# Kernel tuning notes

Measured on AMD Instinct MI355X. Metric: run time of the kernel, lower is better.

The kernel has to match this reference:

```python
import jax, jax.numpy as jnp
import numpy as np

B, S, D, H, DFF = 8, 1024, 1024, 16, 4096
DK = D // H
EPS = 1e-6
NEG = -1e9


def setup_inputs() -> dict:
    key = jax.random.key(0)
    ks = jax.random.split(key, 8)
    x = jax.random.normal(ks[0], (B, S, D), dtype=jnp.float32)
    mask = jnp.ones((B, 1, 1, S), dtype=jnp.int32)
    s = 0.02
    wq = jax.random.normal(ks[1], (D, D), jnp.float32) * s
    wk = jax.random.normal(ks[2], (D, D), jnp.float32) * s
    wv = jax.random.normal(ks[3], (D, D), jnp.float32) * s
    wo = jax.random.normal(ks[4], (D, D), jnp.float32) * s
    bq = jnp.zeros((D,), jnp.float32); bk = jnp.zeros((D,), jnp.float32)
    bv = jnp.zeros((D,), jnp.float32); bo = jnp.zeros((D,), jnp.float32)
    w1 = jax.random.normal(ks[5], (D, DFF), jnp.float32) * s
    b1 = jnp.zeros((DFF,), jnp.float32)
    w2 = jax.random.normal(ks[6], (DFF, D), jnp.float32) * s
    b2 = jnp.zeros((D,), jnp.float32)
    g1 = jnp.array(1.0, jnp.float32); be1 = jnp.array(0.0, jnp.float32)
    g2 = jnp.array(1.0, jnp.float32); be2 = jnp.array(0.0, jnp.float32)
    return dict(x=x, mask=mask, wq=wq, bq=bq, wk=wk, bk=bk, wv=wv, bv=bv,
                wo=wo, bo=bo, w1=w1, b1=b1, w2=w2, b2=b2,
                g1=g1, be1=be1, g2=g2, be2=be2)


def layer_norm(x, gamma, beta):
    # repo quirk: unbiased std (ddof=1), scalar gamma/beta, divide by (std+eps)
    mean = jnp.mean(x, axis=-1, keepdims=True)
    std = jnp.std(x, axis=-1, keepdims=True, ddof=1)
    return gamma * (x - mean) / (std + EPS) + beta


def mha(x, mask, wq, bq, wk, bk, wv, bv, wo, bo):
    q = (x @ wq + bq).reshape(B, S, H, DK).transpose(0, 2, 1, 3)  # bhsd
    k = (x @ wk + bk).reshape(B, S, H, DK).transpose(0, 2, 1, 3)
    v = (x @ wv + bv).reshape(B, S, H, DK).transpose(0, 2, 1, 3)
    scores = jnp.einsum('bhqd,bhkd->bhqk', q, k) / jnp.sqrt(jnp.float32(DK))
    scores = jnp.where(mask == 0, NEG, scores)
    attn = jax.nn.softmax(scores, axis=-1)
    out = jnp.einsum('bhqk,bhkd->bhqd', attn, v)
    out = out.transpose(0, 2, 1, 3).reshape(B, S, D)
    return out @ wo + bo


def reference(x, mask, wq, bq, wk, bk, wv, bv, wo, bo, w1, b1, w2, b2, g1, be1, g2, be2):
    # pre-LN residual: x + sublayer(norm(x)); dropout inert at eval
    x = x + mha(layer_norm(x, g1, be1), mask, wq, bq, wk, bk, wv, bv, wo, bo)
    h = layer_norm(x, g2, be2)
    x = x + (jax.nn.relu(h @ w1 + b1) @ w2 + b2)
    return x
```

## Files before the change

### kernel.cpp

```cpp
#include <hip/hip_runtime.h>
#include <math.h>

typedef __bf16 bf16;
typedef float f32x4 __attribute__((ext_vector_type(4)));
typedef float f32x16 __attribute__((ext_vector_type(16)));
typedef bf16 bf16x8 __attribute__((ext_vector_type(8)));
typedef bf16 bf16x4 __attribute__((ext_vector_type(4)));
typedef unsigned int u32;
typedef unsigned int u32x2 __attribute__((ext_vector_type(2)));

#define DEV __device__ __forceinline__

constexpr int Ss = 1024, Dd = 1024;
constexpr float EPSf = 1e-6f;
constexpr float SM_SCALE = 0.125f * 1.4426950408889634f;

DEV void gl_lds16(const void* g, void* l) {
  __builtin_amdgcn_global_load_lds(
      (const __attribute__((address_space(1))) void*)g,
      (__attribute__((address_space(3))) void*)l, 16, 0, 0);
}

DEV u32 cvtpk(float lo, float hi) {
  u32 r;
  asm("v_cvt_pk_bf16_f32 %0, %1, %2" : "=v"(r) : "v"(lo), "v"(hi));
  return r;
}

__global__ __launch_bounds__(256) void prep_k(
    const float* __restrict__ i0, const float* __restrict__ i1,
    const float* __restrict__ i2, const float* __restrict__ i3,
    const float* __restrict__ i4, const float* __restrict__ i5,
    bf16* __restrict__ o0, bf16* __restrict__ o1, bf16* __restrict__ o2,
    bf16* __restrict__ o3, bf16* __restrict__ o4, bf16* __restrict__ o5,
    const float* __restrict__ xin, bf16* __restrict__ lnout,
    const float* __restrict__ gp, const float* __restrict__ bp) {
  const int bi = blockIdx.x;
  const int tid = threadIdx.x;
  if (bi >= 3072) {
    const int row = bi - 3072;
    float v[4];
    const float* p = xin + (size_t)row * Dd + tid * 4;
#pragma unroll
    for (int i = 0; i < 4; i++) v[i] = p[i];
    float s = v[0] + v[1] + v[2] + v[3];
    float s2 = v[0] * v[0] + v[1] * v[1] + v[2] * v[2] + v[3] * v[3];
#pragma unroll
    for (int m = 1; m < 64; m <<= 1) {
      s += __shfl_xor(s, m, 64);
      s2 += __shfl_xor(s2, m, 64);
    }
    __shared__ float ls[4], ls2[4];
    if ((tid & 63) == 0) {
      ls[tid >> 6] = s;
      ls2[tid >> 6] = s2;
    }
    __syncthreads();
    s = ls[0] + ls[1] + ls[2] + ls[3];
    s2 = ls2[0] + ls2[1] + ls2[2] + ls2[3];
    float mean = s * (1.0f / Dd);
    float var = (s2 - (float)Dd * mean * mean) * (1.0f / (Dd - 1));
    var = fmaxf(var, 0.0f);
    float g = gp[0], be = bp[0];
    float rs = g / (sqrtf(var) + EPSf);
    bf16* q = lnout + (size_t)row * Dd + tid * 4;
#pragma unroll
    for (int i = 0; i < 4; i++) q[i] = (bf16)((v[i] - mean) * rs + be);
    return;
  }
  __shared__ float t[64 * 65];
  const float* in;
  bf16* out;
  int R, C, local, sh;
  if (bi < 1024) {
    const int j = bi >> 8;
    local = bi & 255; R = 1024; C = 1024; sh = 4;
    in = (j == 0) ? i0 : (j == 1) ? i1 : (j == 2) ? i2 : i3;
    out = (j == 0) ? o0 : (j == 1) ? o1 : (j == 2) ? o2 : o3;
  } else if (bi < 2048) {
    local = bi - 1024; R = 1024; C = 4096; sh = 6; in = i4; out = o4;
  } else {
    local = bi - 2048; R = 4096; C = 1024; sh = 4; in = i5; out = o5;
  }
  const int nx = 1 << sh;
  const int bx = local & (nx - 1), by = local >> sh;
  const int tx = tid & 63, ty = tid >> 6;
  const int r0 = by * 64, c0 = bx * 64;
#pragma unroll
  for (int i = 0; i < 16; i++) {
    int r = ty + i * 4;
    t[r * 65 + tx] = in[(size_t)(r0 + r) * C + c0 + tx];
  }
  __syncthreads();
#pragma unroll
  for (int i = 0; i < 16; i++) {
    int r = ty + i * 4;
    out[(size_t)(c0 + r) * R + r0 + tx] = (bf16)t[tx * 65 + r];
  }
}

__global__ __launch_bounds__(256) void ln_bf16_k(
    const bf16* __restrict__ in, bf16* __restrict__ out,
    const float* __restrict__ gp, const float* __restrict__ bp) {
  const int row = blockIdx.x;
  const int tid = threadIdx.x;
  const bf16x4 vv = *(const bf16x4*)(in + (size_t)row * Dd + tid * 4);
  float v[4];
#pragma unroll
  for (int i = 0; i < 4; i++) v[i] = (float)vv[i];
  float s = v[0] + v[1] + v[2] + v[3];
  float s2 = v[0] * v[0] + v[1] * v[1] + v[2] * v[2] + v[3] * v[3];
#pragma unroll
  for (int m = 1; m < 64; m <<= 1) {
    s += __shfl_xor(s, m, 64);
    s2 += __shfl_xor(s2, m, 64);
  }
  __shared__ float ls[4], ls2[4];
  if ((tid & 63) == 0) {
    ls[tid >> 6] = s;
    ls2[tid >> 6] = s2;
  }
  __syncthreads();
  s = ls[0] + ls[1] + ls[2] + ls[3];
  s2 = ls2[0] + ls2[1] + ls2[2] + ls2[3];
  float mean = s * (1.0f / Dd);
  float var = (s2 - (float)Dd * mean * mean) * (1.0f / (Dd - 1));
  var = fmaxf(var, 0.0f);
  float g = gp[0], be = bp[0];
  float rs = g / (sqrtf(var) + EPSf);
  bf16* q = out + (size_t)row * Dd + tid * 4;
#pragma unroll
  for (int i = 0; i < 4; i++) q[i] = (bf16)((v[i] - mean) * rs + be);
}

template <int EPI, int BK>
__global__ __launch_bounds__(256) void gemm_bt(
    const bf16* __restrict__ A, const bf16* __restrict__ Bt,
    const float* __restrict__ bias, const float* __restrict__ bias2,
    const float* __restrict__ bias3, const float* __restrict__ resid,
    const bf16* __restrict__ vtbr, bf16* __restrict__ vtb,
    void* __restrict__ Cout, int M, int N, int K, int sa, int sb) {
  __shared__ __attribute__((aligned(16))) char smem[2 * 128 * BK * 2];
  bf16* As = (bf16*)smem;
  bf16* Bs = (bf16*)(smem + 128 * BK * 2);
  constexpr int CPR = BK / 8;
  constexpr int RPJ = 256 / CPR;
  constexpr int NJ = BK / 16;
  const int tid = threadIdx.x;
  const int ln = tid & 63;
  const int wv = tid >> 6;
  const int wm = wv >> 1, wn = wv & 1;
  const int quad = ln >> 4, l16 = ln & 15;
  const int l7 = l16 & 7;
  const int nxg = gridDim.x;
  const int d = blockIdx.y * nxg + blockIdx.x;
  const int sseq = d >> 3;
  const int bxr = sseq % nxg;
  const int byr = (d & 7) + 8 * (sseq / nxg);
  const int m0 = byr * 128, n0 = bxr * 128;

  f32x4 acc[4][4];
#pragma unroll
  for (int i = 0; i < 4; i++)
#pragma unroll
    for (int j = 0; j < 4; j++) acc[i][j] = {0.f, 0.f, 0.f, 0.f};

  const int sr = tid / CPR;
  const int sc = (tid & (CPR - 1)) ^ (sr & 7);
  const size_t abase = (size_t)(m0 + sr) * sa + sc * 8;
  const size_t bbase = (size_t)(n0 + sr) * sb + sc * 8;

  for (int k0 = 0; k0 < K; k0 += BK) {
#pragma unroll
    for (int j = 0; j < NJ; j++) {
      gl_lds16(A + abase + (size_t)(j * RPJ) * sa + k0,
               (char*)As + j * 4096 + wv * 1024);
      gl_lds16(Bt + bbase + (size_t)(j * RPJ) * sb + k0,
               (char*)Bs + j * 4096 + wv * 1024);
    }
    __syncthreads();
#pragma unroll
    for (int kh = 0; kh < BK / 32; kh++) {
      bf16x8 af[4], bfr[4];
#pragma unroll
      for (int mi = 0; mi < 4; mi++)
        af[mi] = *(const bf16x8*)&As[(wm * 64 + mi * 16 + l16) * BK +
                                     ((kh * 4 + quad) ^ l7) * 8];
#pragma unroll
      for (int ni = 0; ni < 4; ni++)
        bfr[ni] = *(const bf16x8*)&Bs[(wn * 64 + ni * 16 + l16) * BK +
                                      ((kh * 4 + quad) ^ l7) * 8];
#pragma unroll
      for (int mi = 0; mi < 4; mi++)
#pragma unroll
        for (int ni = 0; ni < 4; ni++)
          acc[mi][ni] = __builtin_amdgcn_mfma_f32_16x16x32_bf16(
              af[mi], bfr[ni], acc[mi][ni], 0, 0, 0);
    }
    __syncthreads();
  }

  if constexpr (EPI == 4) {
    if (n0 < 2048) {
#pragma unroll
      for (int mi = 0; mi < 4; mi++) {
        const int m = m0 + wm * 64 + mi * 16 + quad * 4;
#pragma unroll
        for (int ni = 0; ni < 4; ni++) {
          const int n = n0 + wn * 64 + ni * 16 + l16;
          const float bvl = (n < 1024) ? bias[n] : bias2[n - 1024];
#pragma unroll
          for (int r = 0; r < 4; r++)
            ((bf16*)Cout)[(size_t)(m + r) * N + n] =
                (bf16)(acc[mi][ni][r] + bvl);
        }
      }
    } else {
      bf16* T = (bf16*)smem;
#pragma unroll
      for (int mi = 0; mi < 4; mi++) {
        const int ml = wm * 64 + mi * 16 + quad * 4;
        const int c = ml >> 3, hf = (ml >> 2) & 1;
#pragma unroll
        for (int ni = 0; ni < 4; ni++) {
          const int nl = wn * 64 + ni * 16 + l16;
          const float bvl = bias3[(n0 - 2048) + nl];
          bf16x4 tv;
#pragma unroll
          for (int r = 0; r < 4; r++) tv[r] = (bf16)(acc[mi][ni][r] + bvl);
          *(bf16x4*)&T[nl * 128 + ((c ^ (nl & 15)) << 3) + (hf << 2)] = tv;
        }
      }
      __syncthreads();
      const size_t vbase =
          ((size_t)(m0 >> 10) * 1024 + (n0 - 2048)) * Ss + (m0 & 1023);
#pragma unroll
      for (int p = 0; p < 8; p++) {
        const int row = p * 16 + (tid >> 4);
        const int k = tid & 15;
        bf16x8 vv = *(const bf16x8*)&T[row * 128 + ((k ^ (row & 15)) << 3)];
        *(bf16x8*)&vtb[vbase + (size_t)row * Ss + k * 8] = vv;
      }
    }
  } else {
#pragma unroll
    for (int mi = 0; mi < 4; mi++) {
      const int m = m0 + wm * 64 + mi * 16 + quad * 4;
#pragma unroll
      for (int ni = 0; ni < 4; ni++) {
        const int n = n0 + wn * 64 + ni * 16 + l16;
        float bvl = 0.0f;
        if constexpr (EPI != 3) bvl = bias[n];
#pragma unroll
        for (int r = 0; r < 4; r++) {
          float val = acc[mi][ni][r] + bvl;
          const size_t idx = (size_t)(m + r) * N + n;
          if constexpr (EPI == 1) {
            ((float*)Cout)[idx] = val + resid[idx];
          } else if constexpr (EPI == 2) {
            ((bf16*)Cout)[idx] = (bf16)fmaxf(val, 0.0f);
          } else if constexpr (EPI == 3) {
            ((float*)Cout)[idx] = val + resid[idx];
          } else if constexpr (EPI == 5) {
            ((bf16*)Cout)[idx] = (bf16)(val + resid[idx]);
          } else {
            ((float*)Cout)[idx] = val + (float)vtbr[idx];
          }
        }
      }
    }
  }
}

__global__ __launch_bounds__(512) void gemm256_relu(
    const bf16* __restrict__ A, const bf16* __restrict__ Bt,
    const float* __restrict__ bias, bf16* __restrict__ Cout, int M, int N,
    int K, int sa, int sb) {
  __shared__ __attribute__((aligned(16))) char smem[131072];
  const int tid = threadIdx.x;
  const int ln = tid & 63;
  const int wv = tid >> 6;
  const int wm = wv >> 2, wn = wv & 3;
  const int quad = ln >> 4, l16 = ln & 15;
  const int l7 = l16 & 7;
  const int nxg = gridDim.x;
  const int d = blockIdx.y * nxg + blockIdx.x;
  const int sseq = d >> 3;
  const int bxr = sseq % nxg;
  const int byr = (d & 7) + 8 * (sseq / nxg);
  const int m0 = byr * 256, n0 = bxr * 256;

  f32x4 acc[8][4];
#pragma unroll
  for (int i = 0; i < 8; i++)
#pragma unroll
    for (int j = 0; j < 4; j++) acc[i][j] = {0.f, 0.f, 0.f, 0.f};

  const int sr = tid >> 3;
  const int sc = (tid & 7) ^ (sr & 7);
  const size_t abase = (size_t)(m0 + sr) * sa + sc * 8;
  const size_t bbase = (size_t)(n0 + sr) * sb + sc * 8;
  const int w8 = tid >> 6;

  const int nt = K >> 6;
  int cur = 0;

  {
#pragma unroll
    for (int j = 0; j < 4; j++) {
      gl_lds16(A + abase + (size_t)(j * 64) * sa,
               smem + j * 8192 + w8 * 1024);
      gl_lds16(Bt + bbase + (size_t)(j * 64) * sb,
               smem + 32768 + j * 8192 + w8 * 1024);
    }
  }
  asm volatile("s_waitcnt vmcnt(0)" ::: "memory");
  __builtin_amdgcn_s_barrier();

  for (int t = 0; t < nt; ++t) {
    const bf16* As = (const bf16*)(smem + cur * 65536);
    const bf16* Bs = (const bf16*)(smem + cur * 65536 + 32768);
    char* ldst = smem + (cur ^ 1) * 65536;
    const bool pf = (t + 1 < nt);
    const int koff = (t + 1) * 64;

    bf16x8 af0[4][2], af1[4][2], bfr[2][2];

#pragma unroll
    for (int mf = 0; mf < 4; mf++)
#pragma unroll
      for (int kh = 0; kh < 2; kh++)
        af0[mf][kh] = *(const bf16x8*)&As[(wm * 128 + mf * 16 + l16) * 64 +
                                          (((kh * 4 + quad) ^ l7) * 8)];
#pragma unroll
    for (int nf = 0; nf < 2; nf++)
#pragma unroll
      for (int kh = 0; kh < 2; kh++)
        bfr[nf][kh] = *(const bf16x8*)&Bs[(wn * 64 + nf * 16 + l16) * 64 +
                                          (((kh * 4 + quad) ^ l7) * 8)];
    if (pf) {
      gl_lds16(Bt + bbase + koff, ldst + 32768 + w8 * 1024);
      gl_lds16(Bt + bbase + (size_t)64 * sb + koff,
               ldst + 32768 + 8192 + w8 * 1024);
    }
    __builtin_amdgcn_s_barrier();
    __builtin_amdgcn_s_setprio(1);
#pragma unroll
    for (int kh = 0; kh < 2; kh++)
#pragma unroll
      for (int mf = 0; mf < 4; mf++)
#pragma unroll
        for (int nf = 0; nf < 2; nf++)
          acc[mf][nf] = __builtin_amdgcn_mfma_f32_16x16x32_bf16(
              af0[mf][kh], bfr[nf][kh], acc[mf][nf], 0, 0, 0);
    __builtin_amdgcn_s_setprio(0);
    if (pf) {
      asm volatile("s_waitcnt vmcnt(2)" ::: "memory");
    } else {
      asm volatile("s_waitcnt vmcnt(0)" ::: "memory");
    }
    __builtin_amdgcn_s_barrier();

#pragma unroll
    for (int mf = 0; mf < 4; mf++)
#pragma unroll
      for (int kh = 0; kh < 2; kh++)
        af1[mf][kh] =
            *(const bf16x8*)&As[(wm * 128 + 64 + mf * 16 + l16) * 64 +
                                (((kh * 4 + quad) ^ l7) * 8)];
    if (pf) {
      gl_lds16(Bt + bbase + (size_t)128 * sb + koff,
               ldst + 32768 + 16384 + w8 * 1024);
      gl_lds16(Bt + bbase + (size_t)192 * sb + koff,
               ldst + 32768 + 24576 + w8 * 1024);
    }
    __builtin_amdgcn_s_barrier();
    __builtin_amdgcn_s_setprio(1);
#pragma unroll
    for (int kh = 0; kh < 2; kh++)
#pragma unroll
      for (int mf = 0; mf < 4; mf++)
#pragma unroll
        for (int nf = 0; nf < 2; nf++)
          acc[4 + mf][nf] = __builtin_amdgcn_mfma_f32_16x16x32_bf16(
              af1[mf][kh], bfr[nf][kh], acc[4 + mf][nf], 0, 0, 0);
    __builtin_amdgcn_s_setprio(0);
    __builtin_amdgcn_s_barrier();

#pragma unroll
    for (int nf = 0; nf < 2; nf++)
#pragma unroll
      for (int kh = 0; kh < 2; kh++)
        bfr[nf][kh] =
            *(const bf16x8*)&Bs[(wn * 64 + 32 + nf * 16 + l16) * 64 +
                                (((kh * 4 + quad) ^ l7) * 8)];
    if (pf) {
      gl_lds16(A + abase + koff, ldst + w8 * 1024);
      gl_lds16(A + abase + (size_t)128 * sa + koff,
               ldst + 16384 + w8 * 1024);
    }
    __builtin_amdgcn_s_barrier();
    __builtin_amdgcn_s_setprio(1);
#pragma unroll
    for (int kh = 0; kh < 2; kh++)
#pragma unroll
      for (int mf = 0; mf < 4; mf++)
#pragma unroll
        for (int nf = 0; nf < 2; nf++)
          acc[4 + mf][2 + nf] = __builtin_amdgcn_mfma_f32_16x16x32_bf16(
              af1[mf][kh], bfr[nf][kh], acc[4 + mf][2 + nf], 0, 0, 0);
    __builtin_amdgcn_s_setprio(0);
    __builtin_amdgcn_s_barrier();

    if (pf) {
      gl_lds16(A + abase + (size_t)64 * sa + koff, ldst + 8192 + w8 * 1024);
      gl_lds16(A + abase + (size_t)192 * sa + koff,
               ldst + 24576 + w8 * 1024);
    }
    __builtin_amdgcn_s_barrier();
    __builtin_amdgcn_s_setprio(1);
#pragma unroll
    for (int kh = 0; kh < 2; kh++)
#pragma unroll
      for (int mf = 0; mf < 4; mf++)
#pragma unroll
        for (int nf = 0; nf < 2; nf++)
          acc[mf][2 + nf] = __builtin_amdgcn_mfma_f32_16x16x32_bf16(
              af0[mf][kh], bfr[nf][kh], acc[mf][2 + nf], 0, 0, 0);
    __builtin_amdgcn_s_setprio(0);
    if (pf) {
      asm volatile("s_waitcnt vmcnt(2)" ::: "memory");
    } else {
      asm volatile("s_waitcnt vmcnt(0)" ::: "memory");
    }
    __builtin_amdgcn_s_barrier();
    cur ^= 1;
  }

#pragma unroll
  for (int mi = 0; mi < 8; mi++) {
    const int m = m0 + wm * 128 + mi * 16 + quad * 4;
#pragma unroll
    for (int ni = 0; ni < 4; ni++) {
      const int n = n0 + wn * 64 + ni * 16 + l16;
      const float bvl = bias[n];
#pragma unroll
      for (int r = 0; r < 4; r++)
        Cout[(size_t)(m + r) * N + n] =
            (bf16)fmaxf(acc[mi][ni][r] + bvl, 0.0f);
    }
  }
}

__global__ __launch_bounds__(256) void attn_k(
    const bf16* __restrict__ qkv, const bf16* __restrict__ vt,
    const int* __restrict__ mask, bf16* __restrict__ ctx) {
  __shared__ __attribute__((aligned(16))) char smem[36864];
  __shared__ int Ft[16];
  bf16* Qs = (bf16*)smem;
  float* Fm = (float*)(smem + 32768);
  const int tid = threadIdx.x;
  const int l = tid & 63, w = tid >> 6;
  const int lq = l & 31, lh = l >> 5;
  const int lq7 = lq & 7;
  const int bh = blockIdx.x;
  const int b = bh >> 4, h = bh & 15;
  const int q0 = blockIdx.y * 128;
  const int sr = tid >> 3;
  const int sc = (tid & 7) ^ (sr & 7);

  if (tid < 16) Ft[tid] = 0;
  {
#pragma unroll
    for (int j = 0; j < 4; j++) {
      const size_t ga =
          (size_t)(b * Ss + q0 + j * 32 + sr) * 3072 + h * 64 + sc * 8;
      gl_lds16(qkv + ga, smem + j * 4096 + w * 1024);
    }
#pragma unroll
    for (int j = 0; j < 2; j++) {
      const size_t ga =
          (size_t)(b * Ss + j * 32 + sr) * 3072 + 1024 + h * 64 + sc * 8;
      gl_lds16(qkv + ga, smem + 16384 + j * 4096 + w * 1024);
      const size_t gv = (size_t)(bh * 64 + j * 32 + sr) * Ss + sc * 8;
      gl_lds16(vt + gv, smem + 24576 + j * 4096 + w * 1024);
    }
  }
  {
    const int4 mv = *(const int4*)&mask[b * Ss + tid * 4];
    const float ninf = -__builtin_inff();
    Fm[tid * 4 + 0] = mv.x ? 0.0f : ninf;
    Fm[tid * 4 + 1] = mv.y ? 0.0f : ninf;
    Fm[tid * 4 + 2] = mv.z ? 0.0f : ninf;
    Fm[tid * 4 + 3] = mv.w ? 0.0f : ninf;
    if (!(mv.x && mv.y && mv.z && mv.w)) atomicOr(&Ft[tid >> 4], 1);
  }
  __syncthreads();

  bf16x8 qf[4];
#pragma unroll
  for (int s = 0; s < 4; s++)
    qf[s] =
        *(const bf16x8*)&Qs[(w * 32 + lq) * 64 + (((s * 2 + lh) ^ lq7) * 8)];
  __syncthreads();

  f32x16 oacc[2];
#pragma unroll
  for (int d = 0; d < 2; d++)
#pragma unroll
    for (int r = 0; r < 16; r++) oacc[d][r] = 0.0f;
  float rsum = 0.0f;

  for (int t = 0; t < 16; ++t) {
    const int kk0 = t * 64;
    if (t + 1 < 16) {
      char* dst = smem + (((t + 1) & 1) ? 0 : 16384);
      const int nk = kk0 + 64;
#pragma unroll
      for (int j = 0; j < 2; j++) {
        const size_t ga =
            (size_t)(b * Ss + nk + j * 32 + sr) * 3072 + 1024 + h * 64 +
            sc * 8;
        gl_lds16(qkv + ga, dst + j * 4096 + w * 1024);
        const size_t gv = (size_t)(bh * 64 + j * 32 + sr) * Ss + nk + sc * 8;
        gl_lds16(vt + gv, dst + 8192 + j * 4096 + w * 1024);
      }
      asm volatile("s_waitcnt vmcnt(4)" ::: "memory");
    } else {
      asm volatile("s_waitcnt vmcnt(0)" ::: "memory");
    }
    __builtin_amdgcn_s_barrier();
    const bf16* Ks = (const bf16*)(smem + ((t & 1) ? 0 : 16384));
    const bf16* Vs = Ks + 4096;

    f32x16 sacc[2];
#pragma unroll
    for (int kb = 0; kb < 2; kb++)
#pragma unroll
      for (int r = 0; r < 16; r++) sacc[kb][r] = 0.0f;

    __builtin_amdgcn_s_setprio(1);
#pragma unroll
    for (int kb = 0; kb < 2; kb++)
#pragma unroll
      for (int s = 0; s < 4; s++) {
        const bf16x8 kf = *(const bf16x8*)&Ks[(kb * 32 + lq) * 64 +
                                              (((s * 2 + lh) ^ lq7) * 8)];
        sacc[kb] = __builtin_amdgcn_mfma_f32_32x32x16_bf16(kf, qf[s],
                                                           sacc[kb], 0, 0, 0);
      }
    __builtin_amdgcn_s_setprio(0);

    if (__builtin_amdgcn_readfirstlane(Ft[t])) {
#pragma unroll
      for (int kb = 0; kb < 2; kb++)
#pragma unroll
        for (int g = 0; g < 4; g++) {
          const f32x4 mv = *(const f32x4*)&Fm[kk0 + kb * 32 + 4 * lh + 8 * g];
#pragma unroll
          for (int j = 0; j < 4; j++)
            sacc[kb][g * 4 + j] = __builtin_amdgcn_exp2f(
                fmaf(sacc[kb][g * 4 + j], SM_SCALE, mv[j]));
        }
    } else {
#pragma unroll
      for (int kb = 0; kb < 2; kb++)
#pragma unroll
        for (int r = 0; r < 16; r++)
          sacc[kb][r] = __builtin_amdgcn_exp2f(sacc[kb][r] * SM_SCALE);
    }
#pragma unroll
    for (int kb = 0; kb < 2; kb++) {
      const float t0 = (sacc[kb][0] + sacc[kb][1]) + (sacc[kb][2] + sacc[kb][3]);
      const float t1 = (sacc[kb][4] + sacc[kb][5]) + (sacc[kb][6] + sacc[kb][7]);
      const float t2 =
          (sacc[kb][8] + sacc[kb][9]) + (sacc[kb][10] + sacc[kb][11]);
      const float t3 =
          (sacc[kb][12] + sacc[kb][13]) + (sacc[kb][14] + sacc[kb][15]);
      rsum += ((t0 + t1) + (t2 + t3));
    }

    __builtin_amdgcn_s_setprio(1);
#pragma unroll
    for (int tt = 0; tt < 4; tt++) {
      const int kb = tt >> 1, rb = (tt & 1) * 8;
      u32 pa = cvtpk(sacc[kb][rb + 0], sacc[kb][rb + 1]);
      u32 pbv = cvtpk(sacc[kb][rb + 2], sacc[kb][rb + 3]);
      u32 pc = cvtpk(sacc[kb][rb + 4], sacc[kb][rb + 5]);
      u32 pd = cvtpk(sacc[kb][rb + 6], sacc[kb][rb + 7]);
      asm("v_permlane32_swap_b32 %0, %1" : "+v"(pa), "+v"(pc));
      asm("v_permlane32_swap_b32 %0, %1" : "+v"(pbv), "+v"(pd));
      union {
        u32 u[4];
        bf16x8 v;
      } pk;
      pk.u[0] = pa;
      pk.u[1] = pbv;
      pk.u[2] = pc;
      pk.u[3] = pd;
      const int vsw = ((tt * 2 + lh) ^ lq7) * 8;
      const bf16x8 vf0 = *(const bf16x8*)&Vs[lq * 64 + vsw];
      const bf16x8 vf1 = *(const bf16x8*)&Vs[(32 + lq) * 64 + vsw];
      oacc[0] =
          __builtin_amdgcn_mfma_f32_32x32x16_bf16(vf0, pk.v, oacc[0], 0, 0, 0);
      oacc[1] =
          __builtin_amdgcn_mfma_f32_32x32x16_bf16(vf1, pk.v, oacc[1], 0, 0, 0);
    }
    __builtin_amdgcn_s_setprio(0);
    asm volatile("s_waitcnt lgkmcnt(0)" ::: "memory");
    __builtin_amdgcn_s_barrier();
  }

  float xs = rsum, ys = rsum;
  asm("v_permlane32_swap_b32 %0, %1" : "+v"(xs), "+v"(ys));
  const float inv = 1.0f / (xs + ys);

  bf16* Tb = (bf16*)(smem + w * 4608);
#pragma unroll
  for (int dblk = 0; dblk < 2; dblk++)
#pragma unroll
    for (int g = 0; g < 4; g++) {
      const u32 lo =
          cvtpk(oacc[dblk][g * 4 + 0] * inv, oacc[dblk][g * 4 + 1] * inv);
      const u32 hi =
          cvtpk(oacc[dblk][g * 4 + 2] * inv, oacc[dblk][g * 4 + 3] * inv);
      u32x2 pr2;
      pr2[0] = lo;
      pr2[1] = hi;
      const int dbase = dblk * 32 + 8 * g + 4 * lh;
      *(u32x2*)&Tb[lq * 72 + dbase] = pr2;
    }
  __syncthreads();
#pragma unroll
  for (int p = 0; p < 4; p++) {
    const int row = p * 8 + (l >> 3);
    const int ch = l & 7;
    const bf16x8 vv = *(const bf16x8*)&Tb[row * 72 + ch * 8];
    *(bf16x8*)&ctx[(size_t)(b * Ss + q0 + w * 32 + row) * Dd + h * 64 +
                   ch * 8] = vv;
  }
}

extern "C" void kernel_launch(void* const* d_in, const int* in_sizes, int n_in,
                              void* d_out, int out_size, void* d_ws,
                              size_t ws_size, hipStream_t stream) {
  (void)in_sizes; (void)n_in; (void)out_size;
  const float* x = (const float*)d_in[0];
  const int* mask = (const int*)d_in[1];
  const float* wq = (const float*)d_in[2];
  const float* bq = (const float*)d_in[3];
  const float* wk = (const float*)d_in[4];
  const float* bk = (const float*)d_in[5];
  const float* wvw = (const float*)d_in[6];
  const float* bv = (const float*)d_in[7];
  const float* wo = (const float*)d_in[8];
  const float* bo = (const float*)d_in[9];
  const float* w1 = (const float*)d_in[10];
  const float* b1 = (const float*)d_in[11];
  const float* w2 = (const float*)d_in[12];
  const float* b2 = (const float*)d_in[13];
  const float* g1 = (const float*)d_in[14];
  const float* be1 = (const float*)d_in[15];
  const float* g2 = (const float*)d_in[16];
  const float* be2 = (const float*)d_in[17];
  float* out = (float*)d_out;

  char* ws = (char*)d_ws;
  const size_t MB = 1024 * 1024;
  bf16* w1T = (bf16*)(ws + 0 * MB);
  bf16* w2T = (bf16*)(ws + 8 * MB);
  bf16* wqkvT = (bf16*)(ws + 16 * MB);
  bf16* woT = (bf16*)(ws + 22 * MB);
  bf16* lnb = (bf16*)(ws + 24 * MB);
  bf16* qkv = (bf16*)(ws + 40 * MB);
  bf16* vtb = (bf16*)(ws + 88 * MB);
  bf16* x1b = (bf16*)(ws + 40 * MB);
  bf16* ctx = lnb;

  dim3 blk(256);
  prep_k<<<3072 + 8192, blk, 0, stream>>>(
      wq, wk, wvw, wo, w1, w2, wqkvT, wqkvT + (size_t)1024 * 1024,
      wqkvT + (size_t)2048 * 1024, woT, w1T, w2T, x, lnb, g1, be1);
  gemm_bt<4, 64><<<dim3(24, 64), blk, 0, stream>>>(
      lnb, wqkvT, bq, bk, bv, nullptr, nullptr, vtb, qkv, 8192, 3072, 1024,
      1024, 1024);
  attn_k<<<dim3(128, 8), blk, 0, stream>>>(qkv, vtb, mask, ctx);
  gemm_bt<5, 128><<<dim3(8, 64), blk, 0, stream>>>(
      ctx, woT, bo, nullptr, nullptr, x, nullptr, nullptr, x1b, 8192, 1024,
      1024, 1024, 1024);
  ln_bf16_k<<<8192, blk, 0, stream>>>(x1b, lnb, g2, be2);

  if (ws_size >= 136 * MB) {
    bf16* mid = (bf16*)(ws + 72 * MB);
    gemm256_relu<<<dim3(16, 32), dim3(512), 0, stream>>>(
        lnb, w1T, b1, mid, 8192, 4096, 1024, 1024, 1024);
    gemm_bt<6, 128><<<dim3(8, 64), blk, 0, stream>>>(
        mid, w2T, b2, nullptr, nullptr, nullptr, x1b, nullptr, out, 8192,
        1024, 4096, 4096, 4096);
  } else {
    bf16* mid = (bf16*)(ws + 72 * MB);
    gemm256_relu<<<dim3(8, 32), dim3(512), 0, stream>>>(
        lnb, w1T, b1, mid, 8192, 2048, 1024, 1024, 1024);
    gemm_bt<6, 128><<<dim3(8, 64), blk, 0, stream>>>(
        mid, w2T, b2, nullptr, nullptr, nullptr, x1b, nullptr, out, 8192,
        1024, 2048, 2048, 4096);
    gemm256_relu<<<dim3(8, 32), dim3(512), 0, stream>>>(
        lnb, w1T + (size_t)2048 * 1024, b1 + 2048, mid, 8192, 2048, 1024,
        1024, 1024);
    gemm_bt<3, 128><<<dim3(8, 64), blk, 0, stream>>>(
        mid, w2T + 2048, nullptr, nullptr, nullptr, out, nullptr, nullptr,
        out, 8192, 1024, 2048, 2048, 4096);
  }
}
```

Measured before the change: 441.0 us.

## Double-buffer LDS in gemm_bt and rebalance prefetch issue in gemm256_relu

gemm_bt now keeps two 32KB LDS stages with BK fixed at 64. It prefetches the next K tile via global_load_lds while computing on the current one, replacing the load-sync-compute-sync loop. The BK=128 launches for the Wo and W2 GEMMs switch to BK=64 to fit this layout. In gemm256_relu the prefetch loads are redistributed across the first three phases, one barrier is removed, and the vmcnt waits are adjusted. This costs 64KB of LDS per block, which may lower occupancy, and BK=64 means more loop iterations.

Result: faster. 417.1 us (-5.4%).

```diff
diff --git a/kernel.cpp b/kernel.cpp
--- a/kernel.cpp
+++ b/kernel.cpp
@@ -140,9 +140,8 @@
     const float* __restrict__ bias3, const float* __restrict__ resid,
     const bf16* __restrict__ vtbr, bf16* __restrict__ vtb,
     void* __restrict__ Cout, int M, int N, int K, int sa, int sb) {
-  __shared__ __attribute__((aligned(16))) char smem[2 * 128 * BK * 2];
-  bf16* As = (bf16*)smem;
-  bf16* Bs = (bf16*)(smem + 128 * BK * 2);
+  static_assert(BK == 64, "dbuf layout assumes BK=64");
+  __shared__ __attribute__((aligned(16))) char smem[65536];
   constexpr int CPR = BK / 8;
   constexpr int RPJ = 256 / CPR;
   constexpr int NJ = BK / 16;
@@ -170,25 +169,50 @@
   const size_t abase = (size_t)(m0 + sr) * sa + sc * 8;
   const size_t bbase = (size_t)(n0 + sr) * sb + sc * 8;
 
-  for (int k0 = 0; k0 < K; k0 += BK) {
+  const int nt = K >> 6;
+  int cur = 0;
+
+  {
 #pragma unroll
     for (int j = 0; j < NJ; j++) {
-      gl_lds16(A + abase + (size_t)(j * RPJ) * sa + k0,
-               (char*)As + j * 4096 + wv * 1024);
-      gl_lds16(Bt + bbase + (size_t)(j * RPJ) * sb + k0,
-               (char*)Bs + j * 4096 + wv * 1024);
-    }
-    __syncthreads();
-#pragma unroll
-    for (int kh = 0; kh < BK / 32; kh++) {
+      gl_lds16(A + abase + (size_t)(j * RPJ) * sa,
+               (char*)smem + j * 4096 + wv * 1024);
+      gl_lds16(Bt + bbase + (size_t)(j * RPJ) * sb,
+               (char*)smem + 16384 + j * 4096 + wv * 1024);
+    }
+  }
+  asm volatile("s_waitcnt vmcnt(0)" ::: "memory");
+  __builtin_amdgcn_s_barrier();
+
+  for (int t = 0; t < nt; ++t) {
+    if (t + 1 < nt) {
+      char* dl = smem + ((cur ^ 1) * 32768);
+      const int koff = (t + 1) * 64;
+#pragma unroll
+      for (int j = 0; j < NJ; j++) {
+        gl_lds16(A + abase + (size_t)(j * RPJ) * sa + koff,
+                 dl + j * 4096 + wv * 1024);
+        gl_lds16(Bt + bbase + (size_t)(j * RPJ) * sb + koff,
+                 dl + 16384 + j * 4096 + wv * 1024);
+      }
+      asm volatile("s_waitcnt vmcnt(8)" ::: "memory");
+    } else {
+      asm volatile("s_waitcnt vmcnt(0)" ::: "memory");
+    }
+    __builtin_amdgcn_s_barrier();
+
+    const bf16* As = (const bf16*)(smem + cur * 32768);
+    const bf16* Bs = (const bf16*)(smem + cur * 32768 + 16384);
+#pragma unroll
+    for (int kh = 0; kh < 2; kh++) {
       bf16x8 af[4], bfr[4];
 #pragma unroll
       for (int mi = 0; mi < 4; mi++)
-        af[mi] = *(const bf16x8*)&As[(wm * 64 + mi * 16 + l16) * BK +
+        af[mi] = *(const bf16x8*)&As[(wm * 64 + mi * 16 + l16) * 64 +
                                      ((kh * 4 + quad) ^ l7) * 8];
 #pragma unroll
       for (int ni = 0; ni < 4; ni++)
-        bfr[ni] = *(const bf16x8*)&Bs[(wn * 64 + ni * 16 + l16) * BK +
+        bfr[ni] = *(const bf16x8*)&Bs[(wn * 64 + ni * 16 + l16) * 64 +
                                       ((kh * 4 + quad) ^ l7) * 8];
 #pragma unroll
       for (int mi = 0; mi < 4; mi++)
@@ -197,7 +221,8 @@
           acc[mi][ni] = __builtin_amdgcn_mfma_f32_16x16x32_bf16(
               af[mi], bfr[ni], acc[mi][ni], 0, 0, 0);
     }
-    __syncthreads();
+    __builtin_amdgcn_s_barrier();
+    cur ^= 1;
   }
 
   if constexpr (EPI == 4) {
@@ -342,6 +367,8 @@
       gl_lds16(Bt + bbase + koff, ldst + 32768 + w8 * 1024);
       gl_lds16(Bt + bbase + (size_t)64 * sb + koff,
                ldst + 32768 + 8192 + w8 * 1024);
+      gl_lds16(Bt + bbase + (size_t)128 * sb + koff,
+               ldst + 32768 + 16384 + w8 * 1024);
     }
     __builtin_amdgcn_s_barrier();
     __builtin_amdgcn_s_setprio(1);
@@ -355,7 +382,7 @@
               af0[mf][kh], bfr[nf][kh], acc[mf][nf], 0, 0, 0);
     __builtin_amdgcn_s_setprio(0);
     if (pf) {
-      asm volatile("s_waitcnt vmcnt(2)" ::: "memory");
+      asm volatile("s_waitcnt vmcnt(3)" ::: "memory");
     } else {
       asm volatile("s_waitcnt vmcnt(0)" ::: "memory");
     }
@@ -369,10 +396,11 @@
             *(const bf16x8*)&As[(wm * 128 + 64 + mf * 16 + l16) * 64 +
                                 (((kh * 4 + quad) ^ l7) * 8)];
     if (pf) {
-      gl_lds16(Bt + bbase + (size_t)128 * sb + koff,
-               ldst + 32768 + 16384 + w8 * 1024);
       gl_lds16(Bt + bbase + (size_t)192 * sb + koff,
                ldst + 32768 + 24576 + w8 * 1024);
+      gl_lds16(A + abase + koff, ldst + w8 * 1024);
+      gl_lds16(A + abase + (size_t)128 * sa + koff,
+               ldst + 16384 + w8 * 1024);
     }
     __builtin_amdgcn_s_barrier();
     __builtin_amdgcn_s_setprio(1);
@@ -395,9 +423,9 @@
             *(const bf16x8*)&Bs[(wn * 64 + 32 + nf * 16 + l16) * 64 +
                                 (((kh * 4 + quad) ^ l7) * 8)];
     if (pf) {
-      gl_lds16(A + abase + koff, ldst + w8 * 1024);
-      gl_lds16(A + abase + (size_t)128 * sa + koff,
-               ldst + 16384 + w8 * 1024);
+      gl_lds16(A + abase + (size_t)64 * sa + koff, ldst + 8192 + w8 * 1024);
+      gl_lds16(A + abase + (size_t)192 * sa + koff,
+               ldst + 24576 + w8 * 1024);
     }
     __builtin_amdgcn_s_barrier();
     __builtin_amdgcn_s_setprio(1);
@@ -412,12 +440,6 @@
     __builtin_amdgcn_s_setprio(0);
     __builtin_amdgcn_s_barrier();
 
-    if (pf) {
-      gl_lds16(A + abase + (size_t)64 * sa + koff, ldst + 8192 + w8 * 1024);
-      gl_lds16(A + abase + (size_t)192 * sa + koff,
-               ldst + 24576 + w8 * 1024);
-    }
-    __builtin_amdgcn_s_barrier();
     __builtin_amdgcn_s_setprio(1);
 #pragma unroll
     for (int kh = 0; kh < 2; kh++)
@@ -685,7 +707,7 @@
       lnb, wqkvT, bq, bk, bv, nullptr, nullptr, vtb, qkv, 8192, 3072, 1024,
       1024, 1024);
   attn_k<<<dim3(128, 8), blk, 0, stream>>>(qkv, vtb, mask, ctx);
-  gemm_bt<5, 128><<<dim3(8, 64), blk, 0, stream>>>(
+  gemm_bt<5, 64><<<dim3(8, 64), blk, 0, stream>>>(
       ctx, woT, bo, nullptr, nullptr, x, nullptr, nullptr, x1b, 8192, 1024,
       1024, 1024, 1024);
   ln_bf16_k<<<8192, blk, 0, stream>>>(x1b, lnb, g2, be2);
@@ -694,20 +716,20 @@
     bf16* mid = (bf16*)(ws + 72 * MB);
     gemm256_relu<<<dim3(16, 32), dim3(512), 0, stream>>>(
         lnb, w1T, b1, mid, 8192, 4096, 1024, 1024, 1024);
-    gemm_bt<6, 128><<<dim3(8, 64), blk, 0, stream>>>(
+    gemm_bt<6, 64><<<dim3(8, 64), blk, 0, stream>>>(
         mid, w2T, b2, nullptr, nullptr, nullptr, x1b, nullptr, out, 8192,
         1024, 4096, 4096, 4096);
   } else {
     bf16* mid = (bf16*)(ws + 72 * MB);
     gemm256_relu<<<dim3(8, 32), dim3(512), 0, stream>>>(
         lnb, w1T, b1, mid, 8192, 2048, 1024, 1024, 1024);
-    gemm_bt<6, 128><<<dim3(8, 64), blk, 0, stream>>>(
+    gemm_bt<6, 64><<<dim3(8, 64), blk, 0, stream>>>(
         mid, w2T, b2, nullptr, nullptr, nullptr, x1b, nullptr, out, 8192,
         1024, 2048, 2048, 4096);
     gemm256_relu<<<dim3(8, 32), dim3(512), 0, stream>>>(
         lnb, w1T + (size_t)2048 * 1024, b1 + 2048, mid, 8192, 2048, 1024,
         1024, 1024);
-    gemm_bt<3, 128><<<dim3(8, 64), blk, 0, stream>>>(
+    gemm_bt<3, 64><<<dim3(8, 64), blk, 0, stream>>>(
         mid, w2T + 2048, nullptr, nullptr, nullptr, out, nullptr, nullptr,
         out, 8192, 1024, 2048, 2048, 4096);
   }
```
